# Kernel tuning notes

Measured on AMD Instinct MI355X. Metric: run time of the kernel, lower is better.

## Reference

```python
import jax, jax.numpy as jnp
import numpy as np

NHEADS = 16
HEAD_DIM = 128
HIDDEN = 2048
SOFTCAP = 50.0
ROPE_BASE = 10000.0
SCALE = 256.0 ** (-0.5)  # hardcoded in original, NOT head_dim**-0.5


def _rope_tables(T, D, dtype):
    inv_freq = 1.0 / (ROPE_BASE ** (jnp.arange(0, D, 2, dtype=jnp.float32) / D))
    pos = jnp.arange(T, dtype=jnp.float32)
    freqs = pos[:, None] * inv_freq[None, :]            # [T, D/2]
    emb = jnp.concatenate([freqs, freqs], axis=-1)      # [T, D]
    # broadcast shape [1, 1, T, D] for (B, H, T, D) q/k
    return jnp.cos(emb)[None, None].astype(dtype), jnp.sin(emb)[None, None].astype(dtype)


def _rotate_half(x):
    x1, x2 = x[..., : x.shape[-1] // 2], x[..., x.shape[-1] // 2:]
    return jnp.concatenate([-x2, x1], axis=-1)


def setup_inputs() -> dict:
    key = jax.random.key(0)
    ks = jax.random.split(key, 5)
    B, T = 1, 4096
    X = jax.random.normal(ks[0], (B, T, HIDDEN), dtype=jnp.float32)
    std = 0.02
    Wq = jax.random.normal(ks[1], (HIDDEN, NHEADS * HEAD_DIM), dtype=jnp.float32) * std
    Wk = jax.random.normal(ks[2], (HIDDEN, NHEADS * HEAD_DIM), dtype=jnp.float32) * std
    Wv = jax.random.normal(ks[3], (HIDDEN, NHEADS * HEAD_DIM), dtype=jnp.float32) * std
    Wo = jax.random.normal(ks[4], (NHEADS * HEAD_DIM, HIDDEN), dtype=jnp.float32) * std
    return {"X": X, "Wq": Wq, "Wk": Wk, "Wv": Wv, "Wo": Wo}


def reference(X, Wq, Wk, Wv, Wo):
    B, T, C = X.shape
    H, D = NHEADS, HEAD_DIM
    # QKV projections -> [B, H, T, D]
    q = (X @ Wq).reshape(B, T, H, D).transpose(0, 2, 1, 3)
    k = (X @ Wk).reshape(B, T, H, D).transpose(0, 2, 1, 3)
    v = (X @ Wv).reshape(B, T, H, D).transpose(0, 2, 1, 3)
    # RoPE
    cos, sin = _rope_tables(T, D, X.dtype)
    q = q * cos + _rotate_half(q) * sin
    k = k * cos + _rotate_half(k) * sin
    # attention logits with tanh softcapping
    att = jnp.einsum("bhqd,bhkd->bhqk", q, k) * SCALE
    att = jnp.tanh(att / SOFTCAP) * SOFTCAP
    causal = jnp.tril(jnp.ones((T, T), dtype=bool))[None, None]
    att = jnp.where(causal, att, -jnp.inf)
    att = jax.nn.softmax(att, axis=-1)
    # dropout is identity (train=False)
    y = jnp.einsum("bhqk,bhkd->bhqd", att, v)
    y = y.transpose(0, 2, 1, 3).reshape(B, T, H * D)
    return y @ Wo
```

## Files before the change

### kernel.cpp

```cpp
#include <hip/hip_runtime.h>
#include <stdint.h>

#define T_SEQ 4096
#define HID   2048
#define NH    16
#define HD    128

typedef __attribute__((ext_vector_type(8))) short short8;
typedef __attribute__((ext_vector_type(4))) short short4v;
typedef __attribute__((ext_vector_type(4))) float f32x4;

typedef __attribute__((address_space(1))) void as1_void;
typedef __attribute__((address_space(3))) void as3_void;

__device__ __forceinline__ unsigned short f2bf(float f){
  unsigned u = __builtin_bit_cast(unsigned, f);
  u += 0x7fffu + ((u >> 16) & 1u);
  return (unsigned short)(u >> 16);
}
__device__ __forceinline__ float bf2f(unsigned short b){
  unsigned u = ((unsigned)b) << 16;
  return __builtin_bit_cast(float, u);
}
__device__ __forceinline__ void gll16(const void* g, void* l){
  __builtin_amdgcn_global_load_lds((as1_void*)(uintptr_t)g,
                                   (as3_void*)(unsigned)(uintptr_t)l, 16, 0, 0);
}

#define VM_WAIT0    asm volatile("s_waitcnt vmcnt(0)" ::: "memory")
#define LGKM_WAIT0  asm volatile("s_waitcnt lgkmcnt(0)" ::: "memory")
__device__ __forceinline__ void barrier_fence(){
  asm volatile("" ::: "memory");
  __builtin_amdgcn_s_barrier();
  asm volatile("" ::: "memory");
}

__global__ __launch_bounds__(256) void conv_x_k(const float* __restrict__ X,
                                                unsigned short* __restrict__ O){
  int i = (blockIdx.x * 256 + threadIdx.x) * 4;
  float4 v = *(const float4*)(X + i);
  short4v o;
  o[0] = (short)f2bf(v.x); o[1] = (short)f2bf(v.y);
  o[2] = (short)f2bf(v.z); o[3] = (short)f2bf(v.w);
  *(short4v*)(O + i) = o;
}

__global__ __launch_bounds__(256) void conv_wt_k(const float* __restrict__ W0,
                                                 const float* __restrict__ W1,
                                                 const float* __restrict__ W2,
                                                 const float* __restrict__ W3,
                                                 unsigned short* __restrict__ Wt){
  const float* W = (blockIdx.z == 0) ? W0 : (blockIdx.z == 1) ? W1
                   : (blockIdx.z == 2) ? W2 : W3;
  unsigned short* out = Wt + (size_t)blockIdx.z * HID * HID;
  __shared__ float tile[32][33];
  const int x = threadIdx.x;
  const int y = threadIdx.y;
  const int k0 = blockIdx.y * 32, n0 = blockIdx.x * 32;
#pragma unroll
  for (int i = 0; i < 4; ++i){
    int r = y * 4 + i;
    tile[r][x] = W[(size_t)(k0 + r) * HID + n0 + x];
  }
  __syncthreads();
#pragma unroll
  for (int i = 0; i < 4; ++i){
    int r = y * 4 + i;
    out[(size_t)(n0 + r) * HID + k0 + x] = f2bf(tile[x][r]);
  }
}

template<int MODE, int NTOT>
__global__ __launch_bounds__(256, 3) void gemm_bt(
    const unsigned short* __restrict__ A,
    const unsigned short* __restrict__ Bt,
    unsigned short* __restrict__ Qb,
    unsigned short* __restrict__ Kb,
    unsigned short* __restrict__ Vt,
    float* __restrict__ Cf)
{
  constexpr int K = HID;
  __shared__ __align__(16) unsigned short lAB[16384];
  unsigned short* lA = lAB;
  unsigned short* lB = lAB + 8192;

  const int tid  = threadIdx.x;
  const int wave = tid >> 6;
  const int lane = tid & 63;
  const int qd   = lane >> 4;
  const int mm   = lane & 15;
  const int m7   = mm & 7;
  const int wm   = wave >> 1;
  const int wn   = wave & 1;
  const int bm   = blockIdx.y * 128;
  const int bn   = blockIdx.x * 128;

  const unsigned short* ga[4];
  const unsigned short* gb[4];
  unsigned short* la[4];
  unsigned short* lbp[4];
#pragma unroll
  for (int i = 0; i < 4; ++i){
    int s0   = (wave * 4 + i) * 64;
    int slot = s0 + lane;
    int row  = slot >> 3;
    int kb   = (slot & 7) ^ (row & 7);
    ga[i]  = A  + (size_t)(bm + row) * K + kb * 8;
    gb[i]  = Bt + (size_t)(bn + row) * K + kb * 8;
    la[i]  = lA + s0 * 8;
    lbp[i] = lB + s0 * 8;
  }

  int abase[4], bbase[4];
#pragma unroll
  for (int t = 0; t < 4; ++t){
    abase[t] = (wm * 64 + t * 16 + mm) * 8;
    bbase[t] = (wn * 64 + t * 16 + mm) * 8;
  }

  const f32x4 fzero = {0.f, 0.f, 0.f, 0.f};
  f32x4 acc[4][4];
#pragma unroll
  for (int i = 0; i < 4; ++i)
#pragma unroll
    for (int j = 0; j < 4; ++j) acc[i][j] = fzero;

  for (int k0 = 0; k0 < K; k0 += 64){
    __syncthreads();
#pragma unroll
    for (int i = 0; i < 4; ++i){
      gll16(ga[i] + k0, la[i]);
      gll16(gb[i] + k0, lbp[i]);
    }
    __syncthreads();
#pragma unroll
    for (int ks = 0; ks < 2; ++ks){
      const int co = (ks * 4 + qd) ^ m7;
      short8 af[4], bfv[4];
#pragma unroll
      for (int t = 0; t < 4; ++t) af[t]  = *(const short8*)(lA + (abase[t] + co) * 8);
#pragma unroll
      for (int t = 0; t < 4; ++t) bfv[t] = *(const short8*)(lB + (bbase[t] + co) * 8);
#pragma unroll
      for (int i = 0; i < 4; ++i)
#pragma unroll
        for (int j = 0; j < 4; ++j)
          acc[i][j] = __builtin_amdgcn_mfma_f32_16x16x32_bf16(af[i], bfv[j], acc[i][j], 0, 0, 0);
    }
  }

  if (MODE == 0 && bn >= 4096){
    __syncthreads();
    unsigned short* lT = lAB;
#pragma unroll
    for (int i = 0; i < 4; ++i){
#pragma unroll
      for (int j = 0; j < 4; ++j){
        const int d_l   = wn * 64 + j * 16 + mm;
        const int chunk = wm * 16 + i * 4 + qd;
        const int ch    = chunk ^ (d_l & 31);
        short4v pk;
#pragma unroll
        for (int r = 0; r < 4; ++r) pk[r] = (short)f2bf(acc[i][j][r]);
        *(short4v*)(lT + d_l * 128 + ch * 4) = pk;
      }
    }
    __syncthreads();
    const int hV = (bn >> 7) - 32;
    const int dd = tid >> 4;
    const int tg = tid & 15;
#pragma unroll
    for (int p = 0; p < 8; ++p){
      const int d_l = p * 16 + dd;
      const int c0  = (tg * 2)     ^ (d_l & 31);
      const int c1  = (tg * 2 + 1) ^ (d_l & 31);
      short4v lo = *(const short4v*)(lT + d_l * 128 + c0 * 4);
      short4v hi = *(const short4v*)(lT + d_l * 128 + c1 * 4);
      short8 ov;
      ov[0] = lo[0]; ov[1] = lo[1]; ov[2] = lo[2]; ov[3] = lo[3];
      ov[4] = hi[0]; ov[5] = hi[1]; ov[6] = hi[2]; ov[7] = hi[3];
      *(short8*)(Vt + ((size_t)(hV * HD + d_l)) * T_SEQ + bm + tg * 8) = ov;
    }
    return;
  }

#pragma unroll
  for (int i = 0; i < 4; ++i){
#pragma unroll
    for (int j = 0; j < 4; ++j){
      const int col = bn + wn * 64 + j * 16 + mm;
#pragma unroll
      for (int r = 0; r < 4; ++r){
        const int row = bm + wm * 64 + i * 16 + qd * 4 + r;
        const float v = acc[i][j][r];
        if (MODE == 0){
          const int nn  = col & 2047;
          const int h   = nn >> 7;
          const int d   = nn & 127;
          const unsigned short bv = f2bf(v);
          if (col < 2048)      Qb[((size_t)h * T_SEQ + row) * HD + d] = bv;
          else                 Kb[((size_t)h * T_SEQ + row) * HD + d] = bv;
        } else {
          Cf[(size_t)row * NTOT + col] = v;
        }
      }
    }
  }
}

__global__ __launch_bounds__(256) void rope_k(unsigned short* __restrict__ Qb,
                                              unsigned short* __restrict__ Kb){
  const int j = threadIdx.x & 63;
  const int t = blockIdx.x * 4 + (threadIdx.x >> 6);
  const int h = blockIdx.y;
  const float fr = (float)t * __expf(-(float)j * (9.210340371976184f / 64.f));
  const float cs = cosf(fr), sn = sinf(fr);
  const size_t base = ((size_t)h * T_SEQ + t) * HD;
  {
    float x1 = bf2f(Qb[base + j]), x2 = bf2f(Qb[base + j + 64]);
    Qb[base + j]      = f2bf(x1 * cs - x2 * sn);
    Qb[base + j + 64] = f2bf(x2 * cs + x1 * sn);
  }
  {
    float x1 = bf2f(Kb[base + j]), x2 = bf2f(Kb[base + j + 64]);
    Kb[base + j]      = f2bf(x1 * cs - x2 * sn);
    Kb[base + j + 64] = f2bf(x2 * cs + x1 * sn);
  }
}

__global__ __launch_bounds__(256, 3) void attn_k(
    const unsigned short* __restrict__ Qb,
    const unsigned short* __restrict__ Kb,
    const unsigned short* __restrict__ Vt,
    unsigned short* __restrict__ Yb)
{
  __shared__ __align__(16) unsigned char smem[41216];
  unsigned short* lK = (unsigned short*)smem;
  unsigned short* lV = (unsigned short*)(smem + 16384);
  unsigned short (*lP)[32][32] = (unsigned short(*)[32][32])(smem + 32768);
  float* lL = (float*)(smem + 40960);
  float* lO = (float*)smem;

  const int tid  = threadIdx.x;
  const int w    = tid >> 6;
  const int rg   = w >> 1;
  const int kg   = w & 1;
  const int lane = tid & 63;
  const int qd   = lane >> 4;
  const int cc   = lane & 15;
  const int cx   = cc & 7;
  const int r8   = lane >> 3, c7 = lane & 7;

  const int b  = blockIdx.x;
  const int h  = b & 15;
  const int tp = 63 - (b >> 4);
  const int qrow0 = tp * 64 + rg * 32;
  const int iters = tp + 1;

  const int ce  = cc ^ qd;
  const int dlt = (ce & 4) ? -32 : 32;
  const unsigned short* gKbp = Kb + ((size_t)h * T_SEQ + w * 16 + qd) * HD + ce * 8;
  const int cV = c7 ^ r8;
  const unsigned short* gVbp = Vt + ((size_t)h * HD + w * 32 + r8) * T_SEQ + cV * 8;

  const int pc0 = (((cc >> 3)    ) ^ qd) * 8 + (cc & 7);
  const int pc1 = (((cc >> 3) + 2) ^ qd) * 8 + (cc & 7);

  const f32x4 fzero = {0.f, 0.f, 0.f, 0.f};
  const float B0 = 0.09016844006f;
  const float B1 = -4.6962728e-8f;
  const float B2 = 2.9351706e-14f;
  const float CLP = 72.134752f;
  short8 onesv;
#pragma unroll
  for (int j = 0; j < 8; ++j) onesv[j] = (short)0x3F80;

  {
    unsigned short* dK = lK + w * 2048;
#pragma unroll
    for (int i = 0; i < 4; ++i)
      gll16(gKbp + (size_t)(i * 4) * HD + ((i & 1) ? dlt : 0), dK + i * 512);
    unsigned short* dV = lV + w * 2048;
#pragma unroll
    for (int i = 0; i < 4; ++i)
      gll16(gVbp + (size_t)i * 8 * T_SEQ, dV + i * 512);
  }

  short8 qf[2][4];
#pragma unroll
  for (int mt = 0; mt < 2; ++mt)
#pragma unroll
    for (int ks = 0; ks < 4; ++ks)
      qf[mt][ks] = *(const short8*)(Qb + ((size_t)h * T_SEQ + qrow0 + mt * 16 + cc) * HD + ks * 32 + qd * 8);

  f32x4 o[2][8];
  f32x4 acc_l[2];
#pragma unroll
  for (int mt = 0; mt < 2; ++mt){
#pragma unroll
    for (int dn = 0; dn < 8; ++dn) o[mt][dn] = fzero;
    acc_l[mt] = fzero;
  }

#pragma unroll 1
  for (int it = 0; it < iters; ++it){
    const int k0 = it * 64;
    VM_WAIT0;
    barrier_fence();

    f32x4 S[2][2];
#pragma unroll
    for (int mt = 0; mt < 2; ++mt)
#pragma unroll
      for (int nt = 0; nt < 2; ++nt) S[mt][nt] = fzero;
    __builtin_amdgcn_s_setprio(1);
#pragma unroll
    for (int nt = 0; nt < 2; ++nt){
      short8 kf[4];
#pragma unroll
      for (int ks = 0; ks < 4; ++ks)
        kf[ks] = *(const short8*)(lK + ((kg * 32 + nt * 16 + cc) * 16 + ((ks * 4 + qd) ^ cx)) * 8);
#pragma unroll
      for (int mt = 0; mt < 2; ++mt)
#pragma unroll
        for (int ks = 0; ks < 4; ++ks)
          S[mt][nt] = __builtin_amdgcn_mfma_f32_16x16x32_bf16(qf[mt][ks], kf[ks], S[mt][nt], 0, 0, 0);
    }
    __builtin_amdgcn_s_setprio(0);

    const bool domask = (it == iters - 1);
#pragma unroll
    for (int mt = 0; mt < 2; ++mt)
#pragma unroll
      for (int nt = 0; nt < 2; ++nt)
#pragma unroll
        for (int r = 0; r < 4; ++r){
          float s = S[mt][nt][r];
          float w2 = s * s;
          float t = fmaf(w2, B2, B1);
          t = fmaf(w2, t, B0);
          float a = s * t;
          a = __builtin_amdgcn_fmed3f(a, -CLP, CLP);
          float p = __builtin_amdgcn_exp2f(a);
          if (domask){
            int col = k0 + kg * 32 + nt * 16 + cc;
            int row = qrow0 + mt * 16 + qd * 4 + r;
            if (col > row) p = 0.f;
          }
          unsigned u = __builtin_bit_cast(unsigned, p);
          lP[w][mt * 16 + qd * 4 + r][nt ? pc1 : pc0] = (unsigned short)(u >> 16);
        }

    short8 pf[2];
#pragma unroll
    for (int mt = 0; mt < 2; ++mt)
      pf[mt] = *(const short8*)(&lP[w][mt * 16 + cc][(qd ^ (cc >> 2)) * 8]);

    __builtin_amdgcn_s_setprio(1);
#pragma unroll
    for (int dn = 0; dn < 8; ++dn){
      short8 vf = *(const short8*)(lV + ((dn * 16 + cc) * 8 + ((kg * 4 + qd) ^ cx)) * 8);
#pragma unroll
      for (int mt = 0; mt < 2; ++mt)
        o[mt][dn] = __builtin_amdgcn_mfma_f32_16x16x32_bf16(pf[mt], vf, o[mt][dn], 0, 0, 0);
    }
#pragma unroll
    for (int mt = 0; mt < 2; ++mt)
      acc_l[mt] = __builtin_amdgcn_mfma_f32_16x16x32_bf16(pf[mt], onesv, acc_l[mt], 0, 0, 0);
    __builtin_amdgcn_s_setprio(0);

    LGKM_WAIT0;
    barrier_fence();

    if (it + 1 < iters){
      const unsigned short* gK = gKbp + (size_t)(k0 + 64) * HD;
      unsigned short* dK = lK + w * 2048;
#pragma unroll
      for (int i = 0; i < 4; ++i)
        gll16(gK + (size_t)(i * 4) * HD + ((i & 1) ? dlt : 0), dK + i * 512);
      const unsigned short* gV = gVbp + (k0 + 64);
      unsigned short* dV = lV + w * 2048;
#pragma unroll
      for (int i = 0; i < 4; ++i)
        gll16(gV + (size_t)i * 8 * T_SEQ, dV + i * 512);
    }
  }

  __syncthreads();
  if (kg == 1){
#pragma unroll
    for (int mt = 0; mt < 2; ++mt){
#pragma unroll
      for (int dn = 0; dn < 8; ++dn)
        *(f32x4*)&lO[(dn * 16 + cc) * 68 + rg * 32 + mt * 16 + qd * 4] = o[mt][dn];
      if (cc == 0){
#pragma unroll
        for (int r = 0; r < 4; ++r)
          lL[rg * 32 + mt * 16 + qd * 4 + r] = acc_l[mt][r];
      }
    }
  }
  __syncthreads();
  if (kg == 0){
#pragma unroll
    for (int mt = 0; mt < 2; ++mt){
      float inv[4];
#pragma unroll
      for (int r = 0; r < 4; ++r){
        float lt = acc_l[mt][r] + lL[rg * 32 + mt * 16 + qd * 4 + r];
        inv[r] = __builtin_amdgcn_rcpf(lt);
      }
#pragma unroll
      for (int dn = 0; dn < 8; ++dn){
        f32x4 oo = o[mt][dn] + *(const f32x4*)&lO[(dn * 16 + cc) * 68 + rg * 32 + mt * 16 + qd * 4];
#pragma unroll
        for (int r = 0; r < 4; ++r){
          int row = qrow0 + mt * 16 + qd * 4 + r;
          Yb[(size_t)row * HID + h * HD + dn * 16 + cc] = f2bf(oo[r] * inv[r]);
        }
      }
    }
  }
}

extern "C" void kernel_launch(void* const* d_in, const int* in_sizes, int n_in,
                              void* d_out, int out_size, void* d_ws, size_t ws_size,
                              hipStream_t stream) {
  const float* X  = (const float*)d_in[0];
  const float* Wq = (const float*)d_in[1];
  const float* Wk = (const float*)d_in[2];
  const float* Wv = (const float*)d_in[3];
  const float* Wo = (const float*)d_in[4];
  float* out = (float*)d_out;

  unsigned short* ws = (unsigned short*)d_ws;
  unsigned short* Xb = ws;
  unsigned short* Wt = ws + (size_t)8  * 1024 * 1024;
  unsigned short* Qb = ws + (size_t)24 * 1024 * 1024;
  unsigned short* Kb = ws + (size_t)32 * 1024 * 1024;
  unsigned short* Vt = ws + (size_t)40 * 1024 * 1024;
  unsigned short* Yb = Xb;

  conv_x_k<<<8192, 256, 0, stream>>>(X, Xb);
  conv_wt_k<<<dim3(64, 64, 4), dim3(32, 8), 0, stream>>>(Wq, Wk, Wv, Wo, Wt);
  gemm_bt<0, 6144><<<dim3(48, 32), 256, 0, stream>>>(Xb, Wt, Qb, Kb, Vt, nullptr);
  rope_k<<<dim3(1024, NH), 256, 0, stream>>>(Qb, Kb);
  attn_k<<<dim3(1024), 256, 0, stream>>>(Qb, Kb, Vt, Yb);
  gemm_bt<1, 2048><<<dim3(16, 32), 256, 0, stream>>>(Yb, Wt + (size_t)6144 * 2048,
                                                     nullptr, nullptr, nullptr, out);
}
```

Baseline: 425.7 us.

## Double-buffer K in LDS and stream V fragments straight into registers

V tiles are now loaded from global memory directly into register fragments, ping-ponging between two register sets, instead of being staged through LDS. K uses two LDS buffers, and the next tile's K and V loads are issued at the start of each iteration. The main loop is unrolled twice through a macro and needs one barrier per iteration instead of two. This aims to hide load latency behind the MFMA work and cut synchronisation. In exchange it uses about 64 more VGPRs under a 3-wave occupancy bound, which risks spills, and it repeats V reads from global memory across row-group waves.

```diff
diff --git a/kernel.cpp b/kernel.cpp
--- a/kernel.cpp
+++ b/kernel.cpp
@@ -27,8 +27,7 @@
                                    (as3_void*)(unsigned)(uintptr_t)l, 16, 0, 0);
 }
 
-#define VM_WAIT0    asm volatile("s_waitcnt vmcnt(0)" ::: "memory")
-#define LGKM_WAIT0  asm volatile("s_waitcnt lgkmcnt(0)" ::: "memory")
+#define VM_WAIT8    asm volatile("s_waitcnt vmcnt(8)" ::: "memory")
 __device__ __forceinline__ void barrier_fence(){
   asm volatile("" ::: "memory");
   __builtin_amdgcn_s_barrier();
@@ -236,7 +235,6 @@
 {
   __shared__ __align__(16) unsigned char smem[41216];
   unsigned short* lK = (unsigned short*)smem;
-  unsigned short* lV = (unsigned short*)(smem + 16384);
   unsigned short (*lP)[32][32] = (unsigned short(*)[32][32])(smem + 32768);
   float* lL = (float*)(smem + 40960);
   float* lO = (float*)smem;
@@ -249,7 +247,6 @@
   const int qd   = lane >> 4;
   const int cc   = lane & 15;
   const int cx   = cc & 7;
-  const int r8   = lane >> 3, c7 = lane & 7;
 
   const int b  = blockIdx.x;
   const int h  = b & 15;
@@ -260,8 +257,8 @@
   const int ce  = cc ^ qd;
   const int dlt = (ce & 4) ? -32 : 32;
   const unsigned short* gKbp = Kb + ((size_t)h * T_SEQ + w * 16 + qd) * HD + ce * 8;
-  const int cV = c7 ^ r8;
-  const unsigned short* gVbp = Vt + ((size_t)h * HD + w * 32 + r8) * T_SEQ + cV * 8;
+
+  const unsigned short* gVf = Vt + ((size_t)h * HD + cc) * T_SEQ + kg * 32 + qd * 8;
 
   const int pc0 = (((cc >> 3)    ) ^ qd) * 8 + (cc & 7);
   const int pc1 = (((cc >> 3) + 2) ^ qd) * 8 + (cc & 7);
@@ -275,15 +272,15 @@
 #pragma unroll
   for (int j = 0; j < 8; ++j) onesv[j] = (short)0x3F80;
 
+  short8 vfA[8], vfB[8];
   {
     unsigned short* dK = lK + w * 2048;
 #pragma unroll
     for (int i = 0; i < 4; ++i)
       gll16(gKbp + (size_t)(i * 4) * HD + ((i & 1) ? dlt : 0), dK + i * 512);
-    unsigned short* dV = lV + w * 2048;
-#pragma unroll
-    for (int i = 0; i < 4; ++i)
-      gll16(gVbp + (size_t)i * 8 * T_SEQ, dV + i * 512);
+#pragma unroll
+    for (int dn = 0; dn < 8; ++dn)
+      vfA[dn] = *(const short8*)(gVf + (size_t)(dn * 16) * T_SEQ);
   }
 
   short8 qf[2][4];
@@ -302,89 +299,97 @@
     acc_l[mt] = fzero;
   }
 
-#pragma unroll 1
-  for (int it = 0; it < iters; ++it){
-    const int k0 = it * 64;
-    VM_WAIT0;
-    barrier_fence();
-
-    f32x4 S[2][2];
-#pragma unroll
-    for (int mt = 0; mt < 2; ++mt)
-#pragma unroll
-      for (int nt = 0; nt < 2; ++nt) S[mt][nt] = fzero;
-    __builtin_amdgcn_s_setprio(1);
-#pragma unroll
-    for (int nt = 0; nt < 2; ++nt){
-      short8 kf[4];
-#pragma unroll
-      for (int ks = 0; ks < 4; ++ks)
-        kf[ks] = *(const short8*)(lK + ((kg * 32 + nt * 16 + cc) * 16 + ((ks * 4 + qd) ^ cx)) * 8);
-#pragma unroll
-      for (int mt = 0; mt < 2; ++mt)
-#pragma unroll
-        for (int ks = 0; ks < 4; ++ks)
-          S[mt][nt] = __builtin_amdgcn_mfma_f32_16x16x32_bf16(qf[mt][ks], kf[ks], S[mt][nt], 0, 0, 0);
-    }
-    __builtin_amdgcn_s_setprio(0);
-
-    const bool domask = (it == iters - 1);
-#pragma unroll
-    for (int mt = 0; mt < 2; ++mt)
-#pragma unroll
-      for (int nt = 0; nt < 2; ++nt)
-#pragma unroll
-        for (int r = 0; r < 4; ++r){
-          float s = S[mt][nt][r];
-          float w2 = s * s;
-          float t = fmaf(w2, B2, B1);
-          t = fmaf(w2, t, B0);
-          float a = s * t;
-          a = __builtin_amdgcn_fmed3f(a, -CLP, CLP);
-          float p = __builtin_amdgcn_exp2f(a);
-          if (domask){
-            int col = k0 + kg * 32 + nt * 16 + cc;
-            int row = qrow0 + mt * 16 + qd * 4 + r;
-            if (col > row) p = 0.f;
-          }
-          unsigned u = __builtin_bit_cast(unsigned, p);
-          lP[w][mt * 16 + qd * 4 + r][nt ? pc1 : pc0] = (unsigned short)(u >> 16);
-        }
-
-    short8 pf[2];
-#pragma unroll
-    for (int mt = 0; mt < 2; ++mt)
-      pf[mt] = *(const short8*)(&lP[w][mt * 16 + cc][(qd ^ (cc >> 2)) * 8]);
-
-    __builtin_amdgcn_s_setprio(1);
-#pragma unroll
-    for (int dn = 0; dn < 8; ++dn){
-      short8 vf = *(const short8*)(lV + ((dn * 16 + cc) * 8 + ((kg * 4 + qd) ^ cx)) * 8);
-#pragma unroll
-      for (int mt = 0; mt < 2; ++mt)
-        o[mt][dn] = __builtin_amdgcn_mfma_f32_16x16x32_bf16(pf[mt], vf, o[mt][dn], 0, 0, 0);
-    }
-#pragma unroll
-    for (int mt = 0; mt < 2; ++mt)
-      acc_l[mt] = __builtin_amdgcn_mfma_f32_16x16x32_bf16(pf[mt], onesv, acc_l[mt], 0, 0, 0);
-    __builtin_amdgcn_s_setprio(0);
-
-    LGKM_WAIT0;
-    barrier_fence();
-
-    if (it + 1 < iters){
-      const unsigned short* gK = gKbp + (size_t)(k0 + 64) * HD;
-      unsigned short* dK = lK + w * 2048;
-#pragma unroll
-      for (int i = 0; i < 4; ++i)
-        gll16(gK + (size_t)(i * 4) * HD + ((i & 1) ? dlt : 0), dK + i * 512);
-      const unsigned short* gV = gVbp + (k0 + 64);
-      unsigned short* dV = lV + w * 2048;
-#pragma unroll
-      for (int i = 0; i < 4; ++i)
-        gll16(gV + (size_t)i * 8 * T_SEQ, dV + i * 512);
-    }
-  }
+  VM_WAIT8;
+
+#define ATTN_BODY(VFC, VFN, RDOFF, WROFF)                                      \
+  {                                                                            \
+    barrier_fence();            \
+    const int k0 = it * 64;                                                    \
+    if (it + 1 < iters){                                                       \
+      const unsigned short* gK = gKbp + (size_t)(k0 + 64) * HD;                \
+      unsigned short* dK = lK + (WROFF) + w * 2048;                            \
+      _Pragma("unroll")                                                        \
+      for (int i = 0; i < 4; ++i)                                              \
+        gll16(gK + (size_t)(i * 4) * HD + ((i & 1) ? dlt : 0), dK + i * 512);  \
+      _Pragma("unroll")                                                        \
+      for (int dn = 0; dn < 8; ++dn)                                           \
+        VFN[dn] = *(const short8*)(gVf + (size_t)(dn * 16) * T_SEQ + k0 + 64); \
+    }                                                                          \
+                        \
+    f32x4 S[2][2];                                                             \
+    _Pragma("unroll")                                                          \
+    for (int mt = 0; mt < 2; ++mt)                                             \
+      _Pragma("unroll")                                                        \
+      for (int nt = 0; nt < 2; ++nt) S[mt][nt] = fzero;                        \
+    __builtin_amdgcn_s_setprio(1);                                             \
+    _Pragma("unroll")                                                          \
+    for (int nt = 0; nt < 2; ++nt){                                            \
+      short8 kf[4];                                                            \
+      _Pragma("unroll")                                                        \
+      for (int ks = 0; ks < 4; ++ks)                                           \
+        kf[ks] = *(const short8*)(lK + (RDOFF) +                               \
+                   ((kg * 32 + nt * 16 + cc) * 16 + ((ks * 4 + qd) ^ cx)) * 8);\
+      _Pragma("unroll")                                                        \
+      for (int mt = 0; mt < 2; ++mt)                                           \
+        _Pragma("unroll")                                                      \
+        for (int ks = 0; ks < 4; ++ks)                                         \
+          S[mt][nt] = __builtin_amdgcn_mfma_f32_16x16x32_bf16(qf[mt][ks],      \
+                        kf[ks], S[mt][nt], 0, 0, 0);                           \
+    }                                                                          \
+    __builtin_amdgcn_s_setprio(0);                                             \
+    const bool domask = (it == iters - 1);                                     \
+    _Pragma("unroll")                                                          \
+    for (int mt = 0; mt < 2; ++mt)                                             \
+      _Pragma("unroll")                                                        \
+      for (int nt = 0; nt < 2; ++nt)                                           \
+        _Pragma("unroll")                                                      \
+        for (int r = 0; r < 4; ++r){                                           \
+          float s = S[mt][nt][r];                                              \
+          float w2 = s * s;                                                    \
+          float t = fmaf(w2, B2, B1);                                          \
+          t = fmaf(w2, t, B0);                                                 \
+          float a = s * t;                                                     \
+          a = __builtin_amdgcn_fmed3f(a, -CLP, CLP);                           \
+          float p = __builtin_amdgcn_exp2f(a);                                 \
+          if (domask){                                                         \
+            int col = k0 + kg * 32 + nt * 16 + cc;                             \
+            int row = qrow0 + mt * 16 + qd * 4 + r;                            \
+            if (col > row) p = 0.f;                                            \
+          }                                                                    \
+          unsigned u = __builtin_bit_cast(unsigned, p);                        \
+          lP[w][mt * 16 + qd * 4 + r][nt ? pc1 : pc0] = (unsigned short)(u >> 16); \
+        }                                                                      \
+               \
+    short8 pf[2];                                                              \
+    _Pragma("unroll")                                                          \
+    for (int mt = 0; mt < 2; ++mt)                                             \
+      pf[mt] = *(const short8*)(&lP[w][mt * 16 + cc][(qd ^ (cc >> 2)) * 8]);   \
+                                \
+    __builtin_amdgcn_s_setprio(1);                                             \
+    _Pragma("unroll")                                                          \
+    for (int dn = 0; dn < 8; ++dn)                                             \
+      _Pragma("unroll")                                                        \
+      for (int mt = 0; mt < 2; ++mt)                                           \
+        o[mt][dn] = __builtin_amdgcn_mfma_f32_16x16x32_bf16(pf[mt], VFC[dn],   \
+                      o[mt][dn], 0, 0, 0);                                     \
+    _Pragma("unroll")                                                          \
+    for (int mt = 0; mt < 2; ++mt)                                             \
+      acc_l[mt] = __builtin_amdgcn_mfma_f32_16x16x32_bf16(pf[mt], onesv,       \
+                    acc_l[mt], 0, 0, 0);                                       \
+    __builtin_amdgcn_s_setprio(0);                                             \
+    VM_WAIT8;         \
+  }
+
+  {
+    int it = 0;
+    while (true){
+      ATTN_BODY(vfA, vfB, 0, 8192);
+      if (++it == iters) break;
+      ATTN_BODY(vfB, vfA, 8192, 0);
+      if (++it == iters) break;
+    }
+  }
+#undef ATTN_BODY
 
   __syncthreads();
   if (kg == 1){
```

Measured after the change: 691.1 us. 62.4% more time.

## Compute transposed S tile to keep P in registers, drop LDS round-trip

Applied to the files above, without the earlier changes.

Swaps the MFMA operands so each lane holds S^T values whose layout matches the A-operand of the PV MFMA. P is then packed to bf16 directly in registers, which removes the LDS write and read of P. The V fragment is gathered with two 8-byte LDS reads to match the new k-index permutation. The freed LDS and the raised launch-bounds occupancy hint (3 to 4 blocks) aim for more resident waves, at the cost of extra V read instructions and possible register pressure.

```diff
diff --git a/kernel.cpp b/kernel.cpp
--- a/kernel.cpp
+++ b/kernel.cpp
@@ -9,6 +9,7 @@
 typedef __attribute__((ext_vector_type(8))) short short8;
 typedef __attribute__((ext_vector_type(4))) short short4v;
 typedef __attribute__((ext_vector_type(4))) float f32x4;
+typedef __attribute__((ext_vector_type(4))) unsigned int uint4v;
 
 typedef __attribute__((address_space(1))) void as1_void;
 typedef __attribute__((address_space(3))) void as3_void;
@@ -21,6 +22,10 @@
 __device__ __forceinline__ float bf2f(unsigned short b){
   unsigned u = ((unsigned)b) << 16;
   return __builtin_bit_cast(float, u);
+}
+__device__ __forceinline__ unsigned pk2(float a, float b){
+  return (__builtin_bit_cast(unsigned, a) >> 16) |
+         (__builtin_bit_cast(unsigned, b) & 0xffff0000u);
 }
 __device__ __forceinline__ void gll16(const void* g, void* l){
   __builtin_amdgcn_global_load_lds((as1_void*)(uintptr_t)g,
@@ -228,18 +233,17 @@
   }
 }
 
-__global__ __launch_bounds__(256, 3) void attn_k(
+__global__ __launch_bounds__(256, 4) void attn_k(
     const unsigned short* __restrict__ Qb,
     const unsigned short* __restrict__ Kb,
     const unsigned short* __restrict__ Vt,
     unsigned short* __restrict__ Yb)
 {
-  __shared__ __align__(16) unsigned char smem[41216];
+  __shared__ __align__(16) unsigned char smem[35072];
   unsigned short* lK = (unsigned short*)smem;
   unsigned short* lV = (unsigned short*)(smem + 16384);
-  unsigned short (*lP)[32][32] = (unsigned short(*)[32][32])(smem + 32768);
-  float* lL = (float*)(smem + 40960);
   float* lO = (float*)smem;
+  float* lL = (float*)(smem + 34816);
 
   const int tid  = threadIdx.x;
   const int w    = tid >> 6;
@@ -263,8 +267,8 @@
   const int cV = c7 ^ r8;
   const unsigned short* gVbp = Vt + ((size_t)h * HD + w * 32 + r8) * T_SEQ + cV * 8;
 
-  const int pc0 = (((cc >> 3)    ) ^ qd) * 8 + (cc & 7);
-  const int pc1 = (((cc >> 3) + 2) ^ qd) * 8 + (cc & 7);
+  const int cgA = kg * 4 + (qd >> 1);
+  const int vhalf = (qd & 1) * 4;
 
   const f32x4 fzero = {0.f, 0.f, 0.f, 0.f};
   const float B0 = 0.09016844006f;
@@ -308,11 +312,11 @@
     VM_WAIT0;
     barrier_fence();
 
-    f32x4 S[2][2];
-#pragma unroll
-    for (int mt = 0; mt < 2; ++mt)
-#pragma unroll
-      for (int nt = 0; nt < 2; ++nt) S[mt][nt] = fzero;
+    f32x4 St[2][2];
+#pragma unroll
+    for (int nt = 0; nt < 2; ++nt)
+#pragma unroll
+      for (int mt = 0; mt < 2; ++mt) St[nt][mt] = fzero;
     __builtin_amdgcn_s_setprio(1);
 #pragma unroll
     for (int nt = 0; nt < 2; ++nt){
@@ -324,18 +328,20 @@
       for (int mt = 0; mt < 2; ++mt)
 #pragma unroll
         for (int ks = 0; ks < 4; ++ks)
-          S[mt][nt] = __builtin_amdgcn_mfma_f32_16x16x32_bf16(qf[mt][ks], kf[ks], S[mt][nt], 0, 0, 0);
+          St[nt][mt] = __builtin_amdgcn_mfma_f32_16x16x32_bf16(kf[ks], qf[mt][ks], St[nt][mt], 0, 0, 0);
     }
     __builtin_amdgcn_s_setprio(0);
 
     const bool domask = (it == iters - 1);
-#pragma unroll
-    for (int mt = 0; mt < 2; ++mt)
+    short8 pf[2];
+#pragma unroll
+    for (int mt = 0; mt < 2; ++mt){
+      float pv[2][4];
 #pragma unroll
       for (int nt = 0; nt < 2; ++nt)
 #pragma unroll
         for (int r = 0; r < 4; ++r){
-          float s = S[mt][nt][r];
+          float s = St[nt][mt][r];
           float w2 = s * s;
           float t = fmaf(w2, B2, B1);
           t = fmaf(w2, t, B0);
@@ -343,26 +349,32 @@
           a = __builtin_amdgcn_fmed3f(a, -CLP, CLP);
           float p = __builtin_amdgcn_exp2f(a);
           if (domask){
-            int col = k0 + kg * 32 + nt * 16 + cc;
-            int row = qrow0 + mt * 16 + qd * 4 + r;
-            if (col > row) p = 0.f;
+            int key = k0 + kg * 32 + nt * 16 + qd * 4 + r;
+            int row = qrow0 + mt * 16 + cc;
+            if (key > row) p = 0.f;
           }
-          unsigned u = __builtin_bit_cast(unsigned, p);
-          lP[w][mt * 16 + qd * 4 + r][nt ? pc1 : pc0] = (unsigned short)(u >> 16);
+          pv[nt][r] = p;
         }
-
-    short8 pf[2];
-#pragma unroll
-    for (int mt = 0; mt < 2; ++mt)
-      pf[mt] = *(const short8*)(&lP[w][mt * 16 + cc][(qd ^ (cc >> 2)) * 8]);
+      uint4v up;
+      up[0] = pk2(pv[0][0], pv[0][1]);
+      up[1] = pk2(pv[0][2], pv[0][3]);
+      up[2] = pk2(pv[1][0], pv[1][1]);
+      up[3] = pk2(pv[1][2], pv[1][3]);
+      pf[mt] = __builtin_bit_cast(short8, up);
+    }
 
     __builtin_amdgcn_s_setprio(1);
 #pragma unroll
     for (int dn = 0; dn < 8; ++dn){
-      short8 vf = *(const short8*)(lV + ((dn * 16 + cc) * 8 + ((kg * 4 + qd) ^ cx)) * 8);
+      const int drow = (dn * 16 + cc) * 8;
+      short4v vlo = *(const short4v*)(lV + (drow + (cgA ^ cx)) * 8 + vhalf);
+      short4v vhi = *(const short4v*)(lV + (drow + ((cgA + 2) ^ cx)) * 8 + vhalf);
+      short8 vfv;
+      vfv[0] = vlo[0]; vfv[1] = vlo[1]; vfv[2] = vlo[2]; vfv[3] = vlo[3];
+      vfv[4] = vhi[0]; vfv[5] = vhi[1]; vfv[6] = vhi[2]; vfv[7] = vhi[3];
 #pragma unroll
       for (int mt = 0; mt < 2; ++mt)
-        o[mt][dn] = __builtin_amdgcn_mfma_f32_16x16x32_bf16(pf[mt], vf, o[mt][dn], 0, 0, 0);
+        o[mt][dn] = __builtin_amdgcn_mfma_f32_16x16x32_bf16(pf[mt], vfv, o[mt][dn], 0, 0, 0);
     }
 #pragma unroll
     for (int mt = 0; mt < 2; ++mt)
```

Result: slower. 731.7 us (+71.9%).
